# Optimization experiments

Measured on AMD Instinct MI355X. Metric: run time of the kernel, lower is better.

Reference implementation:

```python
import jax, jax.numpy as jnp
import numpy as np
from math import sqrt

SCALE = sqrt(512.0)  # max(key_size, attn_hidden_size, query_size) with scaled=True

def setup_inputs() -> dict:
    key = jax.random.key(0)
    k1, k2, k3, k4, k5 = jax.random.split(key, 5)
    B, T, S, M, N, H = 8, 512, 512, 512, 512, 128
    return {
        "query": jax.random.normal(k1, (B, T, M), dtype=jnp.float32),
        "keys": jax.random.normal(k2, (B, S, N), dtype=jnp.float32),
        "W1": jax.random.normal(k3, (N, H), dtype=jnp.float32),
        "W2": jax.random.normal(k4, (M, H), dtype=jnp.float32),
        "v": jax.random.normal(k5, (H,), dtype=jnp.float32),
    }

def reference(query, keys, W1, W2, v):
    # Project query and keys into attention hidden space
    x1 = jnp.einsum('btm,mh->bth', query, W2)   # (B,T,H)
    x2 = jnp.einsum('bsn,nh->bsh', keys, W1)    # (B,S,H)
    # Broadcast merge (op='add'), tanh activation, v-weighted reduction over H
    merged = jnp.tanh(x1[:, :, None, :] + x2[:, None, :, :])  # (B,T,S,H)
    score = jnp.einsum('btsh,h->bts', merged, v)
    return score / SCALE
```

## Files before the change

### kernel.cpp

```cpp
#include <hip/hip_runtime.h>
#include <hip/hip_fp16.h>


constexpr float SCALE_IN  = 2.8853900817779268f;
constexpr float INV_SCALE = 0.04419417382415922f;

typedef float v2f __attribute__((ext_vector_type(2)));

__device__ __forceinline__ v2f exp2v(v2f z) {
  v2f r;
  r.x = __builtin_amdgcn_exp2f(z.x);
  r.y = __builtin_amdgcn_exp2f(z.y);
  return r;
}
__device__ __forceinline__ v2f rcpv(v2f d) {
  v2f r;
  r.x = __builtin_amdgcn_rcpf(d.x);
  r.y = __builtin_amdgcn_rcpf(d.y);
  return r;
}

__global__ __launch_bounds__(512) void proj_kernel(
    const float* __restrict__ q,  const float* __restrict__ w2,
    const float* __restrict__ ky, const float* __restrict__ w1,
    float* __restrict__ x1z, float* __restrict__ x2z) {
  __shared__ float As[32 * 64];
  __shared__ float Ws[64 * 128];

  int blk = blockIdx.x;
  const float* A; const float* W; float* O;
  if (blk < 128) { A = q;  W = w2; O = x1z; }
  else           { blk -= 128; A = ky; W = w1; O = x2z; }
  const int rbase = blk * 32;
  const int tid = threadIdx.x;

  const int rq = tid >> 5;
  const int hq = tid & 31;

  float acc[2][4];
#pragma unroll
  for (int r = 0; r < 2; ++r)
#pragma unroll
    for (int c = 0; c < 4; ++c) acc[r][c] = 0.0f;

  for (int kb = 0; kb < 512; kb += 64) {
    {
      const int arow = tid >> 4;
      const int kq4  = (tid & 15) * 4;
      *(float4*)(As + arow * 64 + kq4) =
          *(const float4*)(A + (size_t)(rbase + arow) * 512 + kb + kq4);
      const int wrow = tid >> 5;
      const int hq4  = (tid & 31) * 4;
#pragma unroll
      for (int p = 0; p < 4; ++p)
        *(float4*)(Ws + (wrow + 16 * p) * 128 + hq4) =
            *(const float4*)(W + (size_t)(kb + wrow + 16 * p) * 128 + hq4);
    }
    __syncthreads();
#pragma unroll 4
    for (int k4 = 0; k4 < 64; k4 += 4) {
      float a[2][4], w[4][4];
      *(float4*)a[0] = *(const float4*)(As + (2 * rq + 0) * 64 + k4);
      *(float4*)a[1] = *(const float4*)(As + (2 * rq + 1) * 64 + k4);
#pragma unroll
      for (int kk = 0; kk < 4; ++kk)
        *(float4*)w[kk] = *(const float4*)(Ws + (k4 + kk) * 128 + 4 * hq);
#pragma unroll
      for (int kk = 0; kk < 4; ++kk)
#pragma unroll
        for (int r = 0; r < 2; ++r)
#pragma unroll
          for (int c = 0; c < 4; ++c)
            acc[r][c] = fmaf(a[r][kk], w[kk][c], acc[r][c]);
    }
    __syncthreads();
  }

#pragma unroll
  for (int r = 0; r < 2; ++r) {
    float4 z;
    z.x = acc[r][0] * SCALE_IN;
    z.y = acc[r][1] * SCALE_IN;
    z.z = acc[r][2] * SCALE_IN;
    z.w = acc[r][3] * SCALE_IN;
    *(float4*)(O + (size_t)(rbase + 2 * rq + r) * 128 + 4 * hq) = z;
  }
}

__global__ __launch_bounds__(512, 4) void score_kernel(
    const float* __restrict__ x1z, const float* __restrict__ x2z,
    const float* __restrict__ v, float* __restrict__ out) {
  __shared__ float x1l[64 * 64];
  __shared__ float x2l[64 * 64];

  const int tid   = threadIdx.x;
  const int b     = blockIdx.x >> 6;
  const int tile  = blockIdx.x & 63;
  const int tbase = (tile >> 3) * 64;
  const int sbase = (tile & 7) * 64;

  const float* x1g = x1z + (size_t)(b * 512 + tbase) * 128;
  const float* x2g = x2z + (size_t)(b * 512 + sbase) * 128;

  const int sg = tid & 15;
  const int tg = tid >> 4;

  v2f racc[2][2];
#pragma unroll
  for (int i = 0; i < 2; ++i)
#pragma unroll
    for (int jp = 0; jp < 2; ++jp) racc[i][jp] = (v2f){0.0f, 0.0f};
  float sv = 0.0f;

  const v2f C14 = {14.0f, 14.0f};

  for (int ph = 0; ph < 2; ++ph) {
    {
      const int r1 = tid & 63;
      const int c0 = tid >> 6;
#pragma unroll
      for (int p = 0; p < 2; ++p) {
        const int c = c0 + 8 * p;
        const float4 a =
            *(const float4*)(x1g + (size_t)r1 * 128 + ph * 64 + 4 * c);
        x1l[(4 * c + 0) * 64 + r1] = a.x;
        x1l[(4 * c + 1) * 64 + r1] = a.y;
        x1l[(4 * c + 2) * 64 + r1] = a.z;
        x1l[(4 * c + 3) * 64 + r1] = a.w;
        const float4 s =
            *(const float4*)(x2g + (size_t)r1 * 128 + ph * 64 + 4 * c);
        x2l[(4 * c + 0) * 64 + r1] = s.x;
        x2l[(4 * c + 1) * 64 + r1] = s.y;
        x2l[(4 * c + 2) * 64 + r1] = s.z;
        x2l[(4 * c + 3) * 64 + r1] = s.w;
      }
    }
    __syncthreads();

    for (int hg = 0; hg < 8; ++hg) {
      const int h0 = hg * 8;
      const float4 vq0 = *(const float4*)(v + ph * 64 + h0);
      const float4 vq1 = *(const float4*)(v + ph * 64 + h0 + 4);
      sv += (vq0.x + vq0.y) + (vq0.z + vq0.w) +
            (vq1.x + vq1.y) + (vq1.z + vq1.w);

      float zt[2][8];
      v2f   zs[2][8];
#pragma unroll
      for (int qq = 0; qq < 8; ++qq) {
        const float2 tp = *(const float2*)(x1l + (h0 + qq) * 64 + 2 * tg);
        zt[0][qq] = tp.x;
        zt[1][qq] = tp.y;
        const float4 sp = *(const float4*)(x2l + (h0 + qq) * 64 + 4 * sg);
        zs[0][qq] = (v2f){sp.x, sp.y};
        zs[1][qq] = (v2f){sp.z, sp.w};
      }

#pragma unroll
      for (int i = 0; i < 2; ++i) {
#pragma unroll
        for (int jp = 0; jp < 2; ++jp) {
          v2f A[8];
#pragma unroll
          for (int qq = 0; qq < 8; ++qq) {
            const v2f e =
                exp2v(__builtin_elementwise_min(zt[i][qq] + zs[jp][qq], C14));
            A[qq] = e + 1.0f;
          }
          const v2f P01 = A[0] * A[1], P23 = A[2] * A[3];
          const v2f P45 = A[4] * A[5], P67 = A[6] * A[7];
          const v2f P0123 = P01 * P23, P4567 = P45 * P67;
          const v2f D = P0123 * P4567;
          const v2f u01 = vq0.x * A[1] + vq0.y * A[0];
          const v2f u23 = vq0.z * A[3] + vq0.w * A[2];
          const v2f u45 = vq1.x * A[5] + vq1.y * A[4];
          const v2f u67 = vq1.z * A[7] + vq1.w * A[6];
          const v2f n0123 = u01 * P23 + u23 * P01;
          const v2f n4567 = u45 * P67 + u67 * P45;
          const v2f NUM = n0123 * P4567 + n4567 * P0123;
          racc[i][jp] += NUM * rcpv(D);
        }
      }
    }
    __syncthreads();
  }

  const float c1v = sv * INV_SCALE;
  const float c2v = -2.0f * INV_SCALE;
#pragma unroll
  for (int i = 0; i < 2; ++i) {
    const int t = tbase + 2 * tg + i;
    float4 o;
    o.x = fmaf(racc[i][0].x, c2v, c1v);
    o.y = fmaf(racc[i][0].y, c2v, c1v);
    o.z = fmaf(racc[i][1].x, c2v, c1v);
    o.w = fmaf(racc[i][1].y, c2v, c1v);
    *(float4*)(out + (size_t)(b * 512 + t) * 512 + sbase + 4 * sg) = o;
  }
}

extern "C" void kernel_launch(void* const* d_in, const int* in_sizes, int n_in,
                              void* d_out, int out_size, void* d_ws, size_t ws_size,
                              hipStream_t stream) {
  const float* query = (const float*)d_in[0];
  const float* keys  = (const float*)d_in[1];
  const float* W1    = (const float*)d_in[2];
  const float* W2    = (const float*)d_in[3];
  const float* v     = (const float*)d_in[4];
  float* out = (float*)d_out;

  float* x1zp = (float*)d_ws;
  float* x2zp = x1zp + 8 * 512 * 128;

  hipLaunchKernelGGL(proj_kernel, dim3(256), dim3(512), 0, stream,
                     query, W2, keys, W1, x1zp, x2zp);
  hipLaunchKernelGGL(score_kernel, dim3(512), dim3(512), 0, stream,
                     x1zp, x2zp, v, out);
}
```

Before: 138.3 us.

## Split-K projection GEMM with async LDS double buffering and reduce partials in score kernel

The projection kernel now computes a 128-row tile over one quarter of K per block (split-K of four) with 8x4 register tiles. Tiles are staged through double-buffered LDS using global_load_lds direct-to-LDS loads, so the next stage's loads overlap with compute. The four partial planes are summed in the score kernel's shared-memory staging. This raises arithmetic intensity and load/compute overlap in the GEMM, at the cost of writing and rereading four times the intermediate data.

Result: slower. 143.0 us (+3.3%).

```diff
diff --git a/kernel.cpp b/kernel.cpp
--- a/kernel.cpp
+++ b/kernel.cpp
@@ -20,76 +20,104 @@
   return r;
 }
 
+constexpr int PLANE = 4096 * 128;
+
 __global__ __launch_bounds__(512) void proj_kernel(
     const float* __restrict__ q,  const float* __restrict__ w2,
     const float* __restrict__ ky, const float* __restrict__ w1,
-    float* __restrict__ x1z, float* __restrict__ x2z) {
-  __shared__ float As[32 * 64];
-  __shared__ float Ws[64 * 128];
-
-  int blk = blockIdx.x;
-  const float* A; const float* W; float* O;
-  if (blk < 128) { A = q;  W = w2; O = x1z; }
-  else           { blk -= 128; A = ky; W = w1; O = x2z; }
-  const int rbase = blk * 32;
-  const int tid = threadIdx.x;
+    float* __restrict__ part) {
+  __shared__ float lds[2 * 8192];
+
+  const int bid = blockIdx.x;
+  const int mat = bid >> 7;
+  const int rb  = (bid >> 2) & 31;
+  const int ks  = bid & 3;
+  const float* A = mat ? ky : q;
+  const float* W = mat ? w1 : w2;
+  const int rbase = rb * 128;
+  const int k0    = ks * 128;
+
+  const int tid  = threadIdx.x;
+  const int wave = tid >> 6;
+  const int lane = tid & 63;
 
   const int rq = tid >> 5;
   const int hq = tid & 31;
 
-  float acc[2][4];
-#pragma unroll
-  for (int r = 0; r < 2; ++r)
-#pragma unroll
-    for (int c = 0; c < 4; ++c) acc[r][c] = 0.0f;
-
-  for (int kb = 0; kb < 512; kb += 64) {
-    {
-      const int arow = tid >> 4;
-      const int kq4  = (tid & 15) * 4;
-      *(float4*)(As + arow * 64 + kq4) =
-          *(const float4*)(A + (size_t)(rbase + arow) * 512 + kb + kq4);
-      const int wrow = tid >> 5;
-      const int hq4  = (tid & 31) * 4;
-#pragma unroll
-      for (int p = 0; p < 4; ++p)
-        *(float4*)(Ws + (wrow + 16 * p) * 128 + hq4) =
-            *(const float4*)(W + (size_t)(kb + wrow + 16 * p) * 128 + hq4);
+  auto stage = [&](int buf, int ktk) {
+    float* base = lds + buf * 8192;
+    if (wave < 4) {
+#pragma unroll
+      for (int rr = 0; rr < 4; ++rr) {
+        const int cb = wave * 256 + rr * 64;
+        const int c  = cb + lane;
+        const float* src =
+            A + (size_t)(rbase + (c >> 3)) * 512 + ktk + (c & 7) * 4;
+        __builtin_amdgcn_global_load_lds(src, base + cb * 4, 16, 0, 0);
+      }
+    } else {
+#pragma unroll
+      for (int rr = 0; rr < 4; ++rr) {
+        const int cb = (wave - 4) * 256 + rr * 64;
+        const int c  = cb + lane;
+        const float* src =
+            W + (size_t)(ktk + (c >> 5)) * 128 + (c & 31) * 4;
+        __builtin_amdgcn_global_load_lds(src, base + 4096 + cb * 4, 16, 0, 0);
+      }
+    }
+  };
+
+  float4 acc[8];
+#pragma unroll
+  for (int r = 0; r < 8; ++r) acc[r] = make_float4(0.f, 0.f, 0.f, 0.f);
+
+  int buf = 0;
+  stage(0, k0);
+  __syncthreads();
+
+  for (int kt = 0; kt < 4; ++kt) {
+    if (kt < 3) stage(buf ^ 1, k0 + (kt + 1) * 32);
+
+    const float* Ab = lds + buf * 8192;
+    const float* Wb = Ab + 4096;
+#pragma unroll 2
+    for (int k4 = 0; k4 < 32; k4 += 4) {
+      float a[8][4], w[4][4];
+#pragma unroll
+      for (int r = 0; r < 8; ++r)
+        *(float4*)a[r] = *(const float4*)(Ab + (8 * rq + r) * 32 + k4);
+#pragma unroll
+      for (int kk = 0; kk < 4; ++kk)
+        *(float4*)w[kk] = *(const float4*)(Wb + (k4 + kk) * 128 + 4 * hq);
+#pragma unroll
+      for (int kk = 0; kk < 4; ++kk)
+#pragma unroll
+        for (int r = 0; r < 8; ++r) {
+          acc[r].x = fmaf(a[r][kk], w[kk][0], acc[r].x);
+          acc[r].y = fmaf(a[r][kk], w[kk][1], acc[r].y);
+          acc[r].z = fmaf(a[r][kk], w[kk][2], acc[r].z);
+          acc[r].w = fmaf(a[r][kk], w[kk][3], acc[r].w);
+        }
     }
     __syncthreads();
-#pragma unroll 4
-    for (int k4 = 0; k4 < 64; k4 += 4) {
-      float a[2][4], w[4][4];
-      *(float4*)a[0] = *(const float4*)(As + (2 * rq + 0) * 64 + k4);
-      *(float4*)a[1] = *(const float4*)(As + (2 * rq + 1) * 64 + k4);
-#pragma unroll
-      for (int kk = 0; kk < 4; ++kk)
-        *(float4*)w[kk] = *(const float4*)(Ws + (k4 + kk) * 128 + 4 * hq);
-#pragma unroll
-      for (int kk = 0; kk < 4; ++kk)
-#pragma unroll
-        for (int r = 0; r < 2; ++r)
-#pragma unroll
-          for (int c = 0; c < 4; ++c)
-            acc[r][c] = fmaf(a[r][kk], w[kk][c], acc[r][c]);
-    }
-    __syncthreads();
-  }
-
-#pragma unroll
-  for (int r = 0; r < 2; ++r) {
+    buf ^= 1;
+  }
+
+  float* O = part + (size_t)(mat * 4 + ks) * PLANE;
+#pragma unroll
+  for (int r = 0; r < 8; ++r) {
     float4 z;
-    z.x = acc[r][0] * SCALE_IN;
-    z.y = acc[r][1] * SCALE_IN;
-    z.z = acc[r][2] * SCALE_IN;
-    z.w = acc[r][3] * SCALE_IN;
-    *(float4*)(O + (size_t)(rbase + 2 * rq + r) * 128 + 4 * hq) = z;
+    z.x = acc[r].x * SCALE_IN;
+    z.y = acc[r].y * SCALE_IN;
+    z.z = acc[r].z * SCALE_IN;
+    z.w = acc[r].w * SCALE_IN;
+    *(float4*)(O + (size_t)(rbase + 8 * rq + r) * 128 + 4 * hq) = z;
   }
 }
 
 __global__ __launch_bounds__(512, 4) void score_kernel(
-    const float* __restrict__ x1z, const float* __restrict__ x2z,
-    const float* __restrict__ v, float* __restrict__ out) {
+    const float* __restrict__ part, const float* __restrict__ v,
+    float* __restrict__ out) {
   __shared__ float x1l[64 * 64];
   __shared__ float x2l[64 * 64];
 
@@ -99,8 +127,8 @@
   const int tbase = (tile >> 3) * 64;
   const int sbase = (tile & 7) * 64;
 
-  const float* x1g = x1z + (size_t)(b * 512 + tbase) * 128;
-  const float* x2g = x2z + (size_t)(b * 512 + sbase) * 128;
+  const float* x1p = part + (size_t)(b * 512 + tbase) * 128;
+  const float* x2p = part + (size_t)4 * PLANE + (size_t)(b * 512 + sbase) * 128;
 
   const int sg = tid & 15;
   const int tg = tid >> 4;
@@ -121,14 +149,27 @@
 #pragma unroll
       for (int p = 0; p < 2; ++p) {
         const int c = c0 + 8 * p;
-        const float4 a =
-            *(const float4*)(x1g + (size_t)r1 * 128 + ph * 64 + 4 * c);
+        const size_t off = (size_t)r1 * 128 + ph * 64 + 4 * c;
+        float4 a        = *(const float4*)(x1p + off);
+        const float4 a1 = *(const float4*)(x1p + (size_t)PLANE + off);
+        const float4 a2 = *(const float4*)(x1p + (size_t)2 * PLANE + off);
+        const float4 a3 = *(const float4*)(x1p + (size_t)3 * PLANE + off);
+        a.x = (a.x + a1.x) + (a2.x + a3.x);
+        a.y = (a.y + a1.y) + (a2.y + a3.y);
+        a.z = (a.z + a1.z) + (a2.z + a3.z);
+        a.w = (a.w + a1.w) + (a2.w + a3.w);
         x1l[(4 * c + 0) * 64 + r1] = a.x;
         x1l[(4 * c + 1) * 64 + r1] = a.y;
         x1l[(4 * c + 2) * 64 + r1] = a.z;
         x1l[(4 * c + 3) * 64 + r1] = a.w;
-        const float4 s =
-            *(const float4*)(x2g + (size_t)r1 * 128 + ph * 64 + 4 * c);
+        float4 s        = *(const float4*)(x2p + off);
+        const float4 s1 = *(const float4*)(x2p + (size_t)PLANE + off);
+        const float4 s2 = *(const float4*)(x2p + (size_t)2 * PLANE + off);
+        const float4 s3 = *(const float4*)(x2p + (size_t)3 * PLANE + off);
+        s.x = (s.x + s1.x) + (s2.x + s3.x);
+        s.y = (s.y + s1.y) + (s2.y + s3.y);
+        s.z = (s.z + s1.z) + (s2.z + s3.z);
+        s.w = (s.w + s1.w) + (s2.w + s3.w);
         x2l[(4 * c + 0) * 64 + r1] = s.x;
         x2l[(4 * c + 1) * 64 + r1] = s.y;
         x2l[(4 * c + 2) * 64 + r1] = s.z;
@@ -209,11 +250,10 @@
   const float* v     = (const float*)d_in[4];
   float* out = (float*)d_out;
 
-  float* x1zp = (float*)d_ws;
-  float* x2zp = x1zp + 8 * 512 * 128;
+  float* part = (float*)d_ws;
 
   hipLaunchKernelGGL(proj_kernel, dim3(256), dim3(512), 0, stream,
-                     query, W2, keys, W1, x1zp, x2zp);
+                     query, W2, keys, W1, part);
   hipLaunchKernelGGL(score_kernel, dim3(512), dim3(512), 0, stream,
-                     x1zp, x2zp, v, out);
-}
+                     part, v, out);
+}
```
